# Performance work log

Measured on AMD Instinct MI355X. Metric: run time of the kernel, lower is better.

Reference implementation:

```python
import jax, jax.numpy as jnp
import numpy as np

B, T, N, C, H = 8, 96, 1024, 64, 64  # batch, in_len, nodes, hidden_dim, MLP hidden
NUM_TYPES, EMB = 3, 8
GROUPS = 4


def setup_inputs() -> dict:
    key = jax.random.key(0)
    ks = jax.random.split(key, 16)
    s = 0.05
    return {
        "x": jax.random.normal(ks[0], (B, T, 1, N), jnp.float32),
        "adj": jax.random.uniform(ks[1], (N, N), jnp.float32) / N,  # row-normalized-ish
        "node_type": jax.random.randint(ks[2], (N,), 0, NUM_TYPES),
        # input_projection: Conv1d(1, C, 1) -> per-channel scale + bias
        "w_in": jax.random.normal(ks[3], (C,), jnp.float32) * np.sqrt(2.0),
        "b_in": jnp.zeros((C,), jnp.float32),
        # GCN params
        "weights_pool": jax.random.normal(ks[4], (EMB, C, C), jnp.float32) * np.sqrt(2.0 / (EMB + C)),
        "node_emb": jax.random.normal(ks[5], (NUM_TYPES, EMB), jnp.float32) * s,
        # GroupNorm(4, C)
        "gn_w": jnp.ones((C,), jnp.float32),
        "gn_b": jnp.zeros((C,), jnp.float32),
        # ResBlock temporal MLP: Linear(T,H) then Linear(H,T)
        "w1": jax.random.normal(ks[6], (H, T), jnp.float32) * np.sqrt(1.0 / T),
        "b1": jnp.zeros((H,), jnp.float32),
        "w2": jax.random.normal(ks[7], (T, H), jnp.float32) * np.sqrt(1.0 / H),
        "b2": jnp.zeros((T,), jnp.float32),
        # out_projection: Conv1d(C, 1, 1)
        "w_out": jax.random.normal(ks[8], (C,), jnp.float32) * np.sqrt(2.0 / C),
        "b_out": jnp.zeros((), jnp.float32),
    }


def reference(x, adj, node_type, w_in, b_in, weights_pool, node_emb,
              gn_w, gn_b, w1, b1, w2, b2, w_out, b_out):
    Bx, Tx, _, Nx = x.shape
    BT = Bx * Tx
    # input_projection: Conv1d(1->C, k=1) on (BT, 1, N)
    h = x.reshape(BT, Nx)                                   # channel dim is 1
    h = h[:, None, :] * w_in[None, :, None] + b_in[None, :, None]   # (BT, C, N)
    x_in = h
    # --- GCN with adaptive per-node weights ---
    feats = jnp.swapaxes(h, 1, 2)                            # (BT, N, C)
    nt_emb = node_emb[node_type]                             # gather -> (N, 8)
    node_w = jnp.einsum('nd,dio->nio', nt_emb, weights_pool) # (N, C, C)
    feats = jnp.einsum('nm,bmi->bni', adj, feats)            # adj @ feats
    feats = jnp.einsum('bni,nio->bno', feats, node_w)        # per-node matmul
    h = jnp.swapaxes(feats, 1, 2) + x_in                     # (BT, C, N)
    # --- GroupNorm(4, C), eps=1e-5 ---
    g = h.reshape(BT, GROUPS, C // GROUPS, Nx)
    mu = g.mean(axis=(2, 3), keepdims=True)
    var = g.var(axis=(2, 3), keepdims=True)
    g = (g - mu) / jnp.sqrt(var + 1e-5)
    h = g.reshape(BT, C, Nx) * gn_w[None, :, None] + gn_b[None, :, None]
    # --- temporal mixer: (b t) c n -> (b n) t c ---
    h = h.reshape(Bx, Tx, C, Nx).transpose(0, 3, 1, 2).reshape(Bx * Nx, Tx, C)
    ht = jnp.swapaxes(h, 1, 2)                               # (BN, C, T)
    t = jax.nn.relu(ht @ w1.T + b1) @ w2.T + b2              # (BN, C, T)
    h = h + jnp.swapaxes(t, 1, 2)                            # (BN, T, C)
    # --- silu + out_projection: Conv1d(C->1, k=1) over (BN, C, T) ---
    y = jax.nn.silu(jnp.swapaxes(h, 1, 2))                   # (BN, C, T)
    y = jnp.einsum('bct,c->bt', y, w_out) + b_out            # (BN, T)
    y = y.reshape(Bx, Nx, Tx).transpose(0, 2, 1)[:, :, None, :]  # (B, T, 1, N)
    return y
```

## Files before the change

### kernel.cpp

```cpp
#include <hip/hip_runtime.h>
#include <hip/hip_bf16.h>
#include <math.h>

#define B_   8
#define T_   96
#define N_   1024
#define C_   64
#define H_   64
#define BT_  768
#define EMB_ 8

typedef __attribute__((ext_vector_type(8))) short short8v;
typedef __attribute__((ext_vector_type(4))) float f32x4;

__device__ __forceinline__ ushort f2bf(float f) {
    unsigned int u = __float_as_uint(f);
    unsigned int r = (u + 0x7fffu + ((u >> 16) & 1u)) >> 16;
    return (ushort)r;
}
__device__ __forceinline__ float bf2f(ushort h) {
    return __uint_as_float(((unsigned int)h) << 16);
}

__global__ __launch_bounds__(256) void k_setup(const float* __restrict__ wpool,
                                               const float* __restrict__ w_in,
                                               const float* __restrict__ b_in,
                                               const float* __restrict__ adj,
                                               const float* __restrict__ w1,
                                               const float* __restrict__ w2,
                                               float* __restrict__ wp1,
                                               float* __restrict__ wpb,
                                               float* __restrict__ rs,
                                               ushort* __restrict__ wfrag1,
                                               ushort* __restrict__ wfrag2) {
    int bid = blockIdx.x;
    int tid = threadIdx.x;
    if (bid == 0) {
        for (int e = tid; e < EMB_ * C_; e += 256) {
            int d = e >> 6, c = e & 63;
            float s1 = 0.f, s2 = 0.f;
            for (int i = 0; i < C_; ++i) {
                float w = wpool[(d * C_ + i) * C_ + c];
                s1 += w_in[i] * w;
                s2 += b_in[i] * w;
            }
            wp1[e] = s1;
            wpb[e] = s2;
        }
    } else if (bid == 1) {
        for (int e = tid; e < 6144; e += 256) {
            int j = e & 7, lane = (e >> 3) & 63, frag = e >> 9;
            int mt = frag / 3, k0 = frag - 3 * mt;
            int h = 16 * mt + (lane & 15);
            int t = 32 * k0 + 8 * (lane >> 4) + j;
            wfrag1[e] = f2bf(w1[h * T_ + t]);
        }
    } else if (bid == 2) {
        for (int e = tid; e < 6144; e += 256) {
            int j = e & 7, lane = (e >> 3) & 63, frag = e >> 9;
            int mt2 = frag >> 1, ks = frag & 1;
            int t = 16 * mt2 + (lane & 15);
            int h = 32 * ks + 8 * (lane >> 4) + j;
            wfrag2[e] = f2bf(w2[t * H_ + h]);
        }
    } else {
        int row = bid - 3;
        float s = 0.f;
        for (int m = tid; m < N_; m += 256) s += adj[row * N_ + m];
#pragma unroll
        for (int off = 32; off; off >>= 1) s += __shfl_down(s, off);
        __shared__ float red[4];
        if ((tid & 63) == 0) red[tid >> 6] = s;
        __syncthreads();
        if (tid == 0) rs[row] = red[0] + red[1] + red[2] + red[3];
    }
}

__global__ __launch_bounds__(256) void k_tab(const float* __restrict__ wp1,
                                             const float* __restrict__ wpb,
                                             const float* __restrict__ emb,
                                             const float* __restrict__ w_in,
                                             const float* __restrict__ b_in,
                                             float* __restrict__ WT,
                                             float* __restrict__ BTb,
                                             float* __restrict__ TAB,
                                             float* __restrict__ GG) {
    int tid = threadIdx.x;
    int wave = tid >> 6, lane = tid & 63;
    int lq = lane & 15, g = lane >> 4;
    if (wave < 3) {
        int ty = wave, c = lane;
        float w = 0.f, bb = 0.f;
#pragma unroll
        for (int d = 0; d < EMB_; ++d) {
            float ev = emb[ty * EMB_ + d];
            w += ev * wp1[d * C_ + c];
            bb += ev * wpb[d * C_ + c];
        }
        WT[ty * C_ + c] = w;
        BTb[ty * C_ + c] = bb;
        float wi = w_in[c], bi = b_in[c];
        float vals[9] = {w, bb, w * w, bb * bb, w * wi, w * bi, wi * bb, bb * bi, w * bb};
#pragma unroll
        for (int q = 0; q < 9; ++q) {
            vals[q] += __shfl_xor(vals[q], 1);
            vals[q] += __shfl_xor(vals[q], 2);
            vals[q] += __shfl_xor(vals[q], 4);
            vals[q] += __shfl_xor(vals[q], 8);
        }
        if (lq == 0) {
#pragma unroll
            for (int q = 0; q < 9; ++q) TAB[(ty * 4 + g) * 9 + q] = vals[q];
        }
    } else {
        int c = lane;
        float wi = w_in[c], bi = b_in[c];
        float v5[5] = {wi, bi, wi * wi, bi * bi, wi * bi};
#pragma unroll
        for (int q = 0; q < 5; ++q) {
            v5[q] += __shfl_xor(v5[q], 1);
            v5[q] += __shfl_xor(v5[q], 2);
            v5[q] += __shfl_xor(v5[q], 4);
            v5[q] += __shfl_xor(v5[q], 8);
        }
        if (lq == 0) {
#pragma unroll
            for (int q = 0; q < 5; ++q) GG[g * 5 + q] = v5[q];
        }
    }
}

__global__ __launch_bounds__(256, 4) void k_ax(const float* __restrict__ x,
                                               const float* __restrict__ adj,
                                               float* __restrict__ axo) {
    __shared__ ushort Xs[32 * 64];
    __shared__ ushort As[32 * 64];
    const int tid = threadIdx.x;
    const int wave = tid >> 6, lane = tid & 63;
    const int lq = lane & 15, g4 = lane >> 4;
    const int n0 = blockIdx.x * 32, m0 = blockIdx.y * 32;
    const int mi = wave >> 1, ni = wave & 1;
    const int sr = tid >> 3, sq = tid & 7;
    const int sqx = sq ^ (sr & 7);
    const int ra = 16 * mi + lq, rb = 16 * ni + lq;

    f32x4 acc = {0.f, 0.f, 0.f, 0.f};

    for (int k0 = 0; k0 < N_; k0 += 64) {
        __syncthreads();
        {
            const float* px = x + (m0 + sr) * N_ + k0 + sq * 8;
            float4 xa = *(const float4*)px;
            float4 xb = *(const float4*)(px + 4);
            union { short8v v; __hip_bfloat162 h[4]; } o;
            o.h[0] = __float22bfloat162_rn(make_float2(xa.x, xa.y));
            o.h[1] = __float22bfloat162_rn(make_float2(xa.z, xa.w));
            o.h[2] = __float22bfloat162_rn(make_float2(xb.x, xb.y));
            o.h[3] = __float22bfloat162_rn(make_float2(xb.z, xb.w));
            *(short8v*)&Xs[sr * 64 + sqx * 8] = o.v;

            const float* pa = adj + (n0 + sr) * N_ + k0 + sq * 8;
            float4 aa = *(const float4*)pa;
            float4 ab = *(const float4*)(pa + 4);
            o.h[0] = __float22bfloat162_rn(make_float2(aa.x, aa.y));
            o.h[1] = __float22bfloat162_rn(make_float2(aa.z, aa.w));
            o.h[2] = __float22bfloat162_rn(make_float2(ab.x, ab.y));
            o.h[3] = __float22bfloat162_rn(make_float2(ab.z, ab.w));
            *(short8v*)&As[sr * 64 + sqx * 8] = o.v;
        }
        __syncthreads();
#pragma unroll
        for (int ks = 0; ks < 2; ++ks) {
            short8v a = *(const short8v*)&Xs[ra * 64 + ((4 * ks + g4) ^ (ra & 7)) * 8];
            short8v bb = *(const short8v*)&As[rb * 64 + ((4 * ks + g4) ^ (rb & 7)) * 8];
            acc = __builtin_amdgcn_mfma_f32_16x16x32_bf16(a, bb, acc, 0, 0, 0);
        }
    }
#pragma unroll
    for (int r = 0; r < 4; ++r)
        axo[(m0 + 16 * mi + 4 * g4 + r) * N_ + n0 + 16 * ni + lq] = acc[r];
}

__global__ __launch_bounds__(256) void k_gn(const float* __restrict__ x,
                                            const float* __restrict__ ax,
                                            const float* __restrict__ rs,
                                            const int* __restrict__ ntype,
                                            const float* __restrict__ TAB,
                                            const float* __restrict__ GG,
                                            float* __restrict__ muT,
                                            float* __restrict__ rgT) {
    int bt = blockIdx.x;
    int tid = threadIdx.x;
    const float* axr = ax + bt * N_;
    const float* xr = x + bt * N_;
    float S[23];
#pragma unroll
    for (int q = 0; q < 23; ++q) S[q] = 0.f;
#pragma unroll
    for (int i = 0; i < 4; ++i) {
        int n = tid + 256 * i;
        float a = axr[n], xv = xr[n], r = rs[n];
        int ty = ntype[n];
        float e0 = (ty == 0) ? 1.f : 0.f;
        float e1 = (ty == 1) ? 1.f : 0.f;
        float e2 = (ty == 2) ? 1.f : 0.f;
        float a2 = a * a, axp = a * xv, ar = a * r, xrr = xv * r, r2 = r * r;
        S[0] += e0 * a;   S[1] += e1 * a;   S[2] += e2 * a;
        S[3] += e0 * r;   S[4] += e1 * r;   S[5] += e2 * r;
        S[6] += e0 * a2;  S[7] += e1 * a2;  S[8] += e2 * a2;
        S[9] += e0 * r2;  S[10] += e1 * r2; S[11] += e2 * r2;
        S[12] += e0 * axp; S[13] += e1 * axp; S[14] += e2 * axp;
        S[15] += e0 * ar; S[16] += e1 * ar; S[17] += e2 * ar;
        S[18] += e0 * xrr; S[19] += e1 * xrr; S[20] += e2 * xrr;
        S[21] += xv;      S[22] += xv * xv;
    }
#pragma unroll
    for (int q = 0; q < 23; ++q) {
#pragma unroll
        for (int off = 32; off; off >>= 1) S[q] += __shfl_down(S[q], off);
    }
    __shared__ float wred[4][23];
    __shared__ float tot[23];
    int wave = tid >> 6, lane = tid & 63;
    if (lane == 0) {
#pragma unroll
        for (int q = 0; q < 23; ++q) wred[wave][q] = S[q];
    }
    __syncthreads();
    if (tid < 23) tot[tid] = wred[0][tid] + wred[1][tid] + wred[2][tid] + wred[3][tid];
    __syncthreads();
    if (tid < 4) {
        int g = tid;
        float M = 0.f, Q = 0.f;
#pragma unroll
        for (int ty = 0; ty < 3; ++ty) {
            const float* tb = TAB + (ty * 4 + g) * 9;
            float A1v = tot[0 + ty], R1v = tot[3 + ty], A2v = tot[6 + ty];
            float R2v = tot[9 + ty], AXv = tot[12 + ty], ARv = tot[15 + ty];
            float XRv = tot[18 + ty];
            M += tb[0] * A1v + tb[1] * R1v;
            Q += tb[2] * A2v + tb[3] * R2v +
                 2.f * (tb[4] * AXv + tb[5] * A1v + tb[6] * XRv + tb[7] * R1v + tb[8] * ARv);
        }
        float Sx = tot[21], Sx2 = tot[22];
        const float* gg = GG + g * 5;
        M += gg[0] * Sx + 1024.f * gg[1];
        Q += gg[2] * Sx2 + 2.f * gg[4] * Sx + 1024.f * gg[3];
        const float inv = 1.f / 16384.f;
        float m = M * inv;
        float v = Q * inv - m * m;
        int b = bt / T_, t = bt - b * T_;
        muT[(b * 4 + g) * T_ + t] = m;
        rgT[(b * 4 + g) * T_ + t] = rsqrtf(v + 1e-5f);
    }
}

__global__ __launch_bounds__(256, 3) void k_main(const float* __restrict__ x,
                                                 const float* __restrict__ ax,
                                                 const float* __restrict__ rs,
                                                 const int* __restrict__ ntype,
                                                 const float* __restrict__ WT,
                                                 const float* __restrict__ BTb,
                                                 const float* __restrict__ muT,
                                                 const float* __restrict__ rgT,
                                                 const float* __restrict__ w_in,
                                                 const float* __restrict__ b_in,
                                                 const float* __restrict__ gn_w,
                                                 const float* __restrict__ gn_b,
                                                 const ushort* __restrict__ wfrag1,
                                                 const ushort* __restrict__ wfrag2,
                                                 const float* __restrict__ b1,
                                                 const float* __restrict__ b2,
                                                 const float* __restrict__ w_out,
                                                 const float* __restrict__ b_out,
                                                 float* __restrict__ out) {
    __shared__ ushort Hs[64 * 104];
    __shared__ ushort Hd[64 * 104];
    __shared__ float axs[96], xs[96];
    __shared__ float musT[4 * 100], rgsT[4 * 100];
    __shared__ float redp[96][4];

    const int tid = threadIdx.x;
    const int n = blockIdx.x;
    const int b = blockIdx.y;
    const int wm = tid >> 6;
    const int lane = tid & 63;
    const int lq = lane & 15;
    const int g4 = lane >> 4;

    short8v w1f[4][3], w2f[6][2];
#pragma unroll
    for (int mt = 0; mt < 4; ++mt)
#pragma unroll
        for (int k0 = 0; k0 < 3; ++k0)
            w1f[mt][k0] = *(const short8v*)(wfrag1 + (((mt * 3 + k0) << 6) + lane) * 8);
#pragma unroll
    for (int mt2 = 0; mt2 < 6; ++mt2)
#pragma unroll
        for (int ks = 0; ks < 2; ++ks)
            w2f[mt2][ks] = *(const short8v*)(wfrag2 + (((mt2 * 2 + ks) << 6) + lane) * 8);

    if (tid < 192) {
        int t = (tid < 96) ? tid : tid - 96;
        float v = (tid < 96) ? ax[(b * T_ + t) * N_ + n] : x[(b * T_ + t) * N_ + n];
        if (tid < 96) axs[t] = v; else xs[t] = v;
    }
    for (int j = tid; j < 384; j += 256) {
        int g = j / 96, t = j - 96 * g;
        musT[g * 100 + t] = muT[b * 384 + j];
        rgsT[g * 100 + t] = rgT[b * 384 + j];
    }
    __syncthreads();

    const int c = 16 * wm + lq;
    const int ty = ntype[n];
    const float rsn = rs[n];
    const float wlc = WT[ty * C_ + c];
    const float blc = BTb[ty * C_ + c];
    const float wic = w_in[c], bic = b_in[c];
    const float gwc = gn_w[c], gbc = gn_b[c];
    const float base = rsn * blc + bic;

    f32x4 acc1[4] = {{0.f, 0.f, 0.f, 0.f}, {0.f, 0.f, 0.f, 0.f},
                     {0.f, 0.f, 0.f, 0.f}, {0.f, 0.f, 0.f, 0.f}};
#pragma unroll
    for (int k0 = 0; k0 < 3; ++k0) {
        int t8 = 32 * k0 + 8 * g4;
        float4 a0 = *(const float4*)&axs[t8];
        float4 a1 = *(const float4*)&axs[t8 + 4];
        float4 x0 = *(const float4*)&xs[t8];
        float4 x1 = *(const float4*)&xs[t8 + 4];
        float4 m0 = *(const float4*)&musT[wm * 100 + t8];
        float4 m1 = *(const float4*)&musT[wm * 100 + t8 + 4];
        float4 r0 = *(const float4*)&rgsT[wm * 100 + t8];
        float4 r1 = *(const float4*)&rgsT[wm * 100 + t8 + 4];
        float vv[8];
        vv[0] = ((a0.x * wlc + x0.x * wic + base) - m0.x) * (r0.x * gwc) + gbc;
        vv[1] = ((a0.y * wlc + x0.y * wic + base) - m0.y) * (r0.y * gwc) + gbc;
        vv[2] = ((a0.z * wlc + x0.z * wic + base) - m0.z) * (r0.z * gwc) + gbc;
        vv[3] = ((a0.w * wlc + x0.w * wic + base) - m0.w) * (r0.w * gwc) + gbc;
        vv[4] = ((a1.x * wlc + x1.x * wic + base) - m1.x) * (r1.x * gwc) + gbc;
        vv[5] = ((a1.y * wlc + x1.y * wic + base) - m1.y) * (r1.y * gwc) + gbc;
        vv[6] = ((a1.z * wlc + x1.z * wic + base) - m1.z) * (r1.z * gwc) + gbc;
        vv[7] = ((a1.w * wlc + x1.w * wic + base) - m1.w) * (r1.w * gwc) + gbc;
        union { short8v v; __hip_bfloat162 h2[4]; } o;
        o.h2[0] = __float22bfloat162_rn(make_float2(vv[0], vv[1]));
        o.h2[1] = __float22bfloat162_rn(make_float2(vv[2], vv[3]));
        o.h2[2] = __float22bfloat162_rn(make_float2(vv[4], vv[5]));
        o.h2[3] = __float22bfloat162_rn(make_float2(vv[6], vv[7]));
        *(short8v*)&Hs[c * 104 + t8] = o.v;
#pragma unroll
        for (int mt = 0; mt < 4; ++mt)
            acc1[mt] = __builtin_amdgcn_mfma_f32_16x16x32_bf16(w1f[mt][k0], o.v, acc1[mt], 0, 0, 0);
    }

#pragma unroll
    for (int mt = 0; mt < 4; ++mt) {
        float4 b1v = *(const float4*)&b1[16 * mt + 4 * g4];
        __hip_bfloat162 p0 = __float22bfloat162_rn(make_float2(
            fmaxf(acc1[mt][0] + b1v.x, 0.f), fmaxf(acc1[mt][1] + b1v.y, 0.f)));
        __hip_bfloat162 p1 = __float22bfloat162_rn(make_float2(
            fmaxf(acc1[mt][2] + b1v.z, 0.f), fmaxf(acc1[mt][3] + b1v.w, 0.f)));
        union { uint2 u; __hip_bfloat162 h2[2]; } w;
        w.h2[0] = p0; w.h2[1] = p1;
        *(uint2*)&Hd[c * 104 + 16 * mt + 4 * g4] = w.u;
    }

    f32x4 acc2[6] = {{0.f, 0.f, 0.f, 0.f}, {0.f, 0.f, 0.f, 0.f},
                     {0.f, 0.f, 0.f, 0.f}, {0.f, 0.f, 0.f, 0.f},
                     {0.f, 0.f, 0.f, 0.f}, {0.f, 0.f, 0.f, 0.f}};
#pragma unroll
    for (int ks = 0; ks < 2; ++ks) {
        short8v af = *(const short8v*)&Hd[c * 104 + 32 * ks + 8 * g4];
#pragma unroll
        for (int mt2 = 0; mt2 < 6; ++mt2)
            acc2[mt2] = __builtin_amdgcn_mfma_f32_16x16x32_bf16(af, w2f[mt2][ks], acc2[mt2], 0, 0, 0);
    }

    float4 wo4 = *(const float4*)&w_out[16 * wm + 4 * g4];
#pragma unroll
    for (int mt2 = 0; mt2 < 6; ++mt2) {
        int tv = 16 * mt2 + lq;
        float bz = b2[tv];
        float pm = 0.f;
#pragma unroll
        for (int r = 0; r < 4; ++r) {
            float res = bf2f(Hs[(16 * wm + 4 * g4 + r) * 104 + tv]);
            float z = res + acc2[mt2][r] + bz;
            float sg = __builtin_amdgcn_rcpf(1.f + __expf(-z));
            pm += z * sg * wo4[r];
        }
        pm += __shfl_xor(pm, 16);
        pm += __shfl_xor(pm, 32);
        if (g4 == 0) redp[tv][wm] = pm;
    }
    __syncthreads();

    if (tid < 96) {
        float4 v = *(const float4*)&redp[tid][0];
        out[(b * T_ + tid) * N_ + n] = v.x + v.y + v.z + v.w + b_out[0];
    }
}

extern "C" void kernel_launch(void* const* d_in, const int* in_sizes, int n_in,
                              void* d_out, int out_size, void* d_ws, size_t ws_size,
                              hipStream_t stream) {
    const float* x     = (const float*)d_in[0];
    const float* adj   = (const float*)d_in[1];
    const int*   ntype = (const int*)d_in[2];
    const float* w_in  = (const float*)d_in[3];
    const float* b_in  = (const float*)d_in[4];
    const float* wpool = (const float*)d_in[5];
    const float* emb   = (const float*)d_in[6];
    const float* gn_w  = (const float*)d_in[7];
    const float* gn_b  = (const float*)d_in[8];
    const float* w1    = (const float*)d_in[9];
    const float* b1    = (const float*)d_in[10];
    const float* w2    = (const float*)d_in[11];
    const float* b2    = (const float*)d_in[12];
    const float* w_out = (const float*)d_in[13];
    const float* b_out = (const float*)d_in[14];
    float* out = (float*)d_out;
    float* ws = (float*)d_ws;

    float* wp1  = ws;
    float* wpb  = ws + 512;
    float* rsv  = ws + 1024;
    float* WT   = ws + 2048;
    float* BTb  = ws + 2240;
    float* TAB  = ws + 2432;
    float* GG   = ws + 2540;
    float* muT  = ws + 2560;
    float* rgT  = ws + 5632;
    ushort* wfrag1 = (ushort*)(ws + 8704);
    ushort* wfrag2 = (ushort*)(ws + 11776);
    float* axb  = ws + 14848;

    k_setup<<<dim3(1027), dim3(256), 0, stream>>>(wpool, w_in, b_in, adj, w1, w2,
                                                  wp1, wpb, rsv, wfrag1, wfrag2);
    k_tab<<<dim3(1), dim3(256), 0, stream>>>(wp1, wpb, emb, w_in, b_in,
                                             WT, BTb, TAB, GG);
    k_ax<<<dim3(32, 24), dim3(256), 0, stream>>>(x, adj, axb);
    k_gn<<<dim3(768), dim3(256), 0, stream>>>(x, axb, rsv, ntype, TAB, GG, muT, rgT);
    k_main<<<dim3(1024, 8), dim3(256), 0, stream>>>(x, axb, rsv, ntype, WT, BTb,
                                                    muT, rgT, w_in, b_in, gn_w, gn_b,
                                                    wfrag1, wfrag2, b1, b2,
                                                    w_out, b_out, out);
}
```

Baseline: 93.94 us.

## Process four nodes per block in k_main using transposed x and AX buffers

```diff
diff --git a/kernel.cpp b/kernel.cpp
--- a/kernel.cpp
+++ b/kernel.cpp
@@ -28,11 +28,13 @@
                                                const float* __restrict__ adj,
                                                const float* __restrict__ w1,
                                                const float* __restrict__ w2,
+                                               const float* __restrict__ x,
                                                float* __restrict__ wp1,
                                                float* __restrict__ wpb,
                                                float* __restrict__ rs,
                                                ushort* __restrict__ wfrag1,
-                                               ushort* __restrict__ wfrag2) {
+                                               ushort* __restrict__ wfrag2,
+                                               float* __restrict__ xT) {
     int bid = blockIdx.x;
     int tid = threadIdx.x;
     if (bid == 0) {
@@ -63,7 +65,7 @@
             int h = 32 * ks + 8 * (lane >> 4) + j;
             wfrag2[e] = f2bf(w2[t * H_ + h]);
         }
-    } else {
+    } else if (bid < 1027) {
         int row = bid - 3;
         float s = 0.f;
         for (int m = tid; m < N_; m += 256) s += adj[row * N_ + m];
@@ -73,6 +75,24 @@
         if ((tid & 63) == 0) red[tid >> 6] = s;
         __syncthreads();
         if (tid == 0) rs[row] = red[0] + red[1] + red[2] + red[3];
+    } else {
+        __shared__ float tile[64][65];
+        int tnum = bid - 1027;
+        int ti = tnum >> 4;
+        int tj = tnum & 15;
+#pragma unroll
+        for (int k = 0; k < 16; ++k) {
+            int idx = tid + 256 * k;
+            int r = idx >> 6, cq = idx & 63;
+            tile[r][cq] = x[(ti * 64 + r) * N_ + tj * 64 + cq];
+        }
+        __syncthreads();
+#pragma unroll
+        for (int k = 0; k < 16; ++k) {
+            int idx = tid + 256 * k;
+            int r = idx >> 6, cq = idx & 63;
+            xT[(tj * 64 + r) * BT_ + ti * 64 + cq] = tile[cq][r];
+        }
     }
 }
 
@@ -132,7 +152,8 @@
 
 __global__ __launch_bounds__(256, 4) void k_ax(const float* __restrict__ x,
                                                const float* __restrict__ adj,
-                                               float* __restrict__ axo) {
+                                               float* __restrict__ axo,
+                                               float* __restrict__ axT) {
     __shared__ ushort Xs[32 * 64];
     __shared__ ushort As[32 * 64];
     const int tid = threadIdx.x;
@@ -179,6 +200,8 @@
 #pragma unroll
     for (int r = 0; r < 4; ++r)
         axo[(m0 + 16 * mi + 4 * g4 + r) * N_ + n0 + 16 * ni + lq] = acc[r];
+    float4 tv = make_float4(acc[0], acc[1], acc[2], acc[3]);
+    *(float4*)&axT[(n0 + 16 * ni + lq) * BT_ + m0 + 16 * mi + 4 * g4] = tv;
 }
 
 __global__ __launch_bounds__(256) void k_gn(const float* __restrict__ x,
@@ -255,8 +278,8 @@
     }
 }
 
-__global__ __launch_bounds__(256, 3) void k_main(const float* __restrict__ x,
-                                                 const float* __restrict__ ax,
+__global__ __launch_bounds__(256, 4) void k_main(const float* __restrict__ xT,
+                                                 const float* __restrict__ axT,
                                                  const float* __restrict__ rs,
                                                  const int* __restrict__ ntype,
                                                  const float* __restrict__ WT,
@@ -276,12 +299,12 @@
                                                  float* __restrict__ out) {
     __shared__ ushort Hs[64 * 104];
     __shared__ ushort Hd[64 * 104];
-    __shared__ float axs[96], xs[96];
+    __shared__ float axs[4][96], xs[4][96];
     __shared__ float musT[4 * 100], rgsT[4 * 100];
-    __shared__ float redp[96][4];
+    __shared__ float redp[4][96][4];
 
     const int tid = threadIdx.x;
-    const int n = blockIdx.x;
+    const int n0 = blockIdx.x * 4;
     const int b = blockIdx.y;
     const int wm = tid >> 6;
     const int lane = tid & 63;
@@ -300,105 +323,122 @@
         for (int ks = 0; ks < 2; ++ks)
             w2f[mt2][ks] = *(const short8v*)(wfrag2 + (((mt2 * 2 + ks) << 6) + lane) * 8);
 
-    if (tid < 192) {
-        int t = (tid < 96) ? tid : tid - 96;
-        float v = (tid < 96) ? ax[(b * T_ + t) * N_ + n] : x[(b * T_ + t) * N_ + n];
-        if (tid < 96) axs[t] = v; else xs[t] = v;
+    for (int j = tid; j < 384; j += 256) {
+        int nn = j / 96, t = j - nn * 96;
+        axs[nn][t] = axT[(n0 + nn) * BT_ + b * T_ + t];
+        xs[nn][t] = xT[(n0 + nn) * BT_ + b * T_ + t];
     }
     for (int j = tid; j < 384; j += 256) {
         int g = j / 96, t = j - 96 * g;
         musT[g * 100 + t] = muT[b * 384 + j];
         rgsT[g * 100 + t] = rgT[b * 384 + j];
     }
-    __syncthreads();
 
     const int c = 16 * wm + lq;
-    const int ty = ntype[n];
-    const float rsn = rs[n];
-    const float wlc = WT[ty * C_ + c];
-    const float blc = BTb[ty * C_ + c];
     const float wic = w_in[c], bic = b_in[c];
     const float gwc = gn_w[c], gbc = gn_b[c];
-    const float base = rsn * blc + bic;
-
-    f32x4 acc1[4] = {{0.f, 0.f, 0.f, 0.f}, {0.f, 0.f, 0.f, 0.f},
-                     {0.f, 0.f, 0.f, 0.f}, {0.f, 0.f, 0.f, 0.f}};
-#pragma unroll
-    for (int k0 = 0; k0 < 3; ++k0) {
-        int t8 = 32 * k0 + 8 * g4;
-        float4 a0 = *(const float4*)&axs[t8];
-        float4 a1 = *(const float4*)&axs[t8 + 4];
-        float4 x0 = *(const float4*)&xs[t8];
-        float4 x1 = *(const float4*)&xs[t8 + 4];
-        float4 m0 = *(const float4*)&musT[wm * 100 + t8];
-        float4 m1 = *(const float4*)&musT[wm * 100 + t8 + 4];
-        float4 r0 = *(const float4*)&rgsT[wm * 100 + t8];
-        float4 r1 = *(const float4*)&rgsT[wm * 100 + t8 + 4];
-        float vv[8];
-        vv[0] = ((a0.x * wlc + x0.x * wic + base) - m0.x) * (r0.x * gwc) + gbc;
-        vv[1] = ((a0.y * wlc + x0.y * wic + base) - m0.y) * (r0.y * gwc) + gbc;
-        vv[2] = ((a0.z * wlc + x0.z * wic + base) - m0.z) * (r0.z * gwc) + gbc;
-        vv[3] = ((a0.w * wlc + x0.w * wic + base) - m0.w) * (r0.w * gwc) + gbc;
-        vv[4] = ((a1.x * wlc + x1.x * wic + base) - m1.x) * (r1.x * gwc) + gbc;
-        vv[5] = ((a1.y * wlc + x1.y * wic + base) - m1.y) * (r1.y * gwc) + gbc;
-        vv[6] = ((a1.z * wlc + x1.z * wic + base) - m1.z) * (r1.z * gwc) + gbc;
-        vv[7] = ((a1.w * wlc + x1.w * wic + base) - m1.w) * (r1.w * gwc) + gbc;
-        union { short8v v; __hip_bfloat162 h2[4]; } o;
-        o.h2[0] = __float22bfloat162_rn(make_float2(vv[0], vv[1]));
-        o.h2[1] = __float22bfloat162_rn(make_float2(vv[2], vv[3]));
-        o.h2[2] = __float22bfloat162_rn(make_float2(vv[4], vv[5]));
-        o.h2[3] = __float22bfloat162_rn(make_float2(vv[6], vv[7]));
-        *(short8v*)&Hs[c * 104 + t8] = o.v;
-#pragma unroll
-        for (int mt = 0; mt < 4; ++mt)
-            acc1[mt] = __builtin_amdgcn_mfma_f32_16x16x32_bf16(w1f[mt][k0], o.v, acc1[mt], 0, 0, 0);
-    }
-
-#pragma unroll
-    for (int mt = 0; mt < 4; ++mt) {
-        float4 b1v = *(const float4*)&b1[16 * mt + 4 * g4];
-        __hip_bfloat162 p0 = __float22bfloat162_rn(make_float2(
-            fmaxf(acc1[mt][0] + b1v.x, 0.f), fmaxf(acc1[mt][1] + b1v.y, 0.f)));
-        __hip_bfloat162 p1 = __float22bfloat162_rn(make_float2(
-            fmaxf(acc1[mt][2] + b1v.z, 0.f), fmaxf(acc1[mt][3] + b1v.w, 0.f)));
-        union { uint2 u; __hip_bfloat162 h2[2]; } w;
-        w.h2[0] = p0; w.h2[1] = p1;
-        *(uint2*)&Hd[c * 104 + 16 * mt + 4 * g4] = w.u;
-    }
-
-    f32x4 acc2[6] = {{0.f, 0.f, 0.f, 0.f}, {0.f, 0.f, 0.f, 0.f},
-                     {0.f, 0.f, 0.f, 0.f}, {0.f, 0.f, 0.f, 0.f},
-                     {0.f, 0.f, 0.f, 0.f}, {0.f, 0.f, 0.f, 0.f}};
-#pragma unroll
-    for (int ks = 0; ks < 2; ++ks) {
-        short8v af = *(const short8v*)&Hd[c * 104 + 32 * ks + 8 * g4];
-#pragma unroll
-        for (int mt2 = 0; mt2 < 6; ++mt2)
-            acc2[mt2] = __builtin_amdgcn_mfma_f32_16x16x32_bf16(af, w2f[mt2][ks], acc2[mt2], 0, 0, 0);
-    }
-
-    float4 wo4 = *(const float4*)&w_out[16 * wm + 4 * g4];
-#pragma unroll
-    for (int mt2 = 0; mt2 < 6; ++mt2) {
-        int tv = 16 * mt2 + lq;
-        float bz = b2[tv];
-        float pm = 0.f;
-#pragma unroll
-        for (int r = 0; r < 4; ++r) {
-            float res = bf2f(Hs[(16 * wm + 4 * g4 + r) * 104 + tv]);
-            float z = res + acc2[mt2][r] + bz;
-            float sg = __builtin_amdgcn_rcpf(1.f + __expf(-z));
-            pm += z * sg * wo4[r];
-        }
-        pm += __shfl_xor(pm, 16);
-        pm += __shfl_xor(pm, 32);
-        if (g4 == 0) redp[tv][wm] = pm;
-    }
+    const float wlcA[3] = {WT[c], WT[64 + c], WT[128 + c]};
+    const float blcA[3] = {BTb[c], BTb[64 + c], BTb[128 + c]};
+    float4 b1q[4];
+#pragma unroll
+    for (int mt = 0; mt < 4; ++mt) b1q[mt] = *(const float4*)&b1[16 * mt + 4 * g4];
+    float b2q[6];
+#pragma unroll
+    for (int mt2 = 0; mt2 < 6; ++mt2) b2q[mt2] = b2[16 * mt2 + lq];
+    const float4 wo4 = *(const float4*)&w_out[16 * wm + 4 * g4];
     __syncthreads();
 
+#pragma unroll 1
+    for (int nn = 0; nn < 4; ++nn) {
+        const int n = n0 + nn;
+        const int ty = ntype[n];
+        const float wlc = (ty == 0) ? wlcA[0] : (ty == 1) ? wlcA[1] : wlcA[2];
+        const float blc = (ty == 0) ? blcA[0] : (ty == 1) ? blcA[1] : blcA[2];
+        const float base = rs[n] * blc + bic;
+
+        f32x4 acc1[4] = {{0.f, 0.f, 0.f, 0.f}, {0.f, 0.f, 0.f, 0.f},
+                         {0.f, 0.f, 0.f, 0.f}, {0.f, 0.f, 0.f, 0.f}};
+#pragma unroll
+        for (int k0 = 0; k0 < 3; ++k0) {
+            int t8 = 32 * k0 + 8 * g4;
+            float4 a0 = *(const float4*)&axs[nn][t8];
+            float4 a1 = *(const float4*)&axs[nn][t8 + 4];
+            float4 x0 = *(const float4*)&xs[nn][t8];
+            float4 x1 = *(const float4*)&xs[nn][t8 + 4];
+            float4 m0 = *(const float4*)&musT[wm * 100 + t8];
+            float4 m1 = *(const float4*)&musT[wm * 100 + t8 + 4];
+            float4 r0 = *(const float4*)&rgsT[wm * 100 + t8];
+            float4 r1 = *(const float4*)&rgsT[wm * 100 + t8 + 4];
+            float vv[8];
+            vv[0] = ((a0.x * wlc + x0.x * wic + base) - m0.x) * (r0.x * gwc) + gbc;
+            vv[1] = ((a0.y * wlc + x0.y * wic + base) - m0.y) * (r0.y * gwc) + gbc;
+            vv[2] = ((a0.z * wlc + x0.z * wic + base) - m0.z) * (r0.z * gwc) + gbc;
+            vv[3] = ((a0.w * wlc + x0.w * wic + base) - m0.w) * (r0.w * gwc) + gbc;
+            vv[4] = ((a1.x * wlc + x1.x * wic + base) - m1.x) * (r1.x * gwc) + gbc;
+            vv[5] = ((a1.y * wlc + x1.y * wic + base) - m1.y) * (r1.y * gwc) + gbc;
+            vv[6] = ((a1.z * wlc + x1.z * wic + base) - m1.z) * (r1.z * gwc) + gbc;
+            vv[7] = ((a1.w * wlc + x1.w * wic + base) - m1.w) * (r1.w * gwc) + gbc;
+            union { short8v v; __hip_bfloat162 h2[4]; } o;
+            o.h2[0] = __float22bfloat162_rn(make_float2(vv[0], vv[1]));
+            o.h2[1] = __float22bfloat162_rn(make_float2(vv[2], vv[3]));
+            o.h2[2] = __float22bfloat162_rn(make_float2(vv[4], vv[5]));
+            o.h2[3] = __float22bfloat162_rn(make_float2(vv[6], vv[7]));
+            *(short8v*)&Hs[c * 104 + t8] = o.v;
+#pragma unroll
+            for (int mt = 0; mt < 4; ++mt)
+                acc1[mt] = __builtin_amdgcn_mfma_f32_16x16x32_bf16(w1f[mt][k0], o.v, acc1[mt], 0, 0, 0);
+        }
+
+#pragma unroll
+        for (int mt = 0; mt < 4; ++mt) {
+            __hip_bfloat162 p0 = __float22bfloat162_rn(make_float2(
+                fmaxf(acc1[mt][0] + b1q[mt].x, 0.f), fmaxf(acc1[mt][1] + b1q[mt].y, 0.f)));
+            __hip_bfloat162 p1 = __float22bfloat162_rn(make_float2(
+                fmaxf(acc1[mt][2] + b1q[mt].z, 0.f), fmaxf(acc1[mt][3] + b1q[mt].w, 0.f)));
+            union { uint2 u; __hip_bfloat162 h2[2]; } w;
+            w.h2[0] = p0; w.h2[1] = p1;
+            *(uint2*)&Hd[c * 104 + 16 * mt + 4 * g4] = w.u;
+        }
+
+        f32x4 acc2[6] = {{0.f, 0.f, 0.f, 0.f}, {0.f, 0.f, 0.f, 0.f},
+                         {0.f, 0.f, 0.f, 0.f}, {0.f, 0.f, 0.f, 0.f},
+                         {0.f, 0.f, 0.f, 0.f}, {0.f, 0.f, 0.f, 0.f}};
+#pragma unroll
+        for (int ks = 0; ks < 2; ++ks) {
+            short8v af = *(const short8v*)&Hd[c * 104 + 32 * ks + 8 * g4];
+#pragma unroll
+            for (int mt2 = 0; mt2 < 6; ++mt2)
+                acc2[mt2] = __builtin_amdgcn_mfma_f32_16x16x32_bf16(af, w2f[mt2][ks], acc2[mt2], 0, 0, 0);
+        }
+
+#pragma unroll
+        for (int mt2 = 0; mt2 < 6; ++mt2) {
+            int tv = 16 * mt2 + lq;
+            float pm = 0.f;
+#pragma unroll
+            for (int r = 0; r < 4; ++r) {
+                float res = bf2f(Hs[(16 * wm + 4 * g4 + r) * 104 + tv]);
+                float z = res + acc2[mt2][r] + b2q[mt2];
+                float sg = __builtin_amdgcn_rcpf(1.f + __expf(-z));
+                pm += z * sg * wo4[r];
+            }
+            pm += __shfl_xor(pm, 16);
+            pm += __shfl_xor(pm, 32);
+            if (g4 == 0) redp[nn][tv][wm] = pm;
+        }
+    }
+    __syncthreads();
+
     if (tid < 96) {
-        float4 v = *(const float4*)&redp[tid][0];
-        out[(b * T_ + tid) * N_ + n] = v.x + v.y + v.z + v.w + b_out[0];
+        float bo = b_out[0];
+        float4 y;
+        float* py = (float*)&y;
+#pragma unroll
+        for (int nn = 0; nn < 4; ++nn) {
+            float4 v = *(const float4*)&redp[nn][tid][0];
+            py[nn] = v.x + v.y + v.z + v.w + bo;
+        }
+        *(float4*)&out[(b * T_ + tid) * N_ + n0] = y;
     }
 }
 
@@ -435,15 +475,17 @@
     ushort* wfrag1 = (ushort*)(ws + 8704);
     ushort* wfrag2 = (ushort*)(ws + 11776);
     float* axb  = ws + 14848;
-
-    k_setup<<<dim3(1027), dim3(256), 0, stream>>>(wpool, w_in, b_in, adj, w1, w2,
-                                                  wp1, wpb, rsv, wfrag1, wfrag2);
+    float* axTb = ws + 14848 + 786432;
+    float* xTb  = ws + 14848 + 2 * 786432;
+
+    k_setup<<<dim3(1219), dim3(256), 0, stream>>>(wpool, w_in, b_in, adj, w1, w2, x,
+                                                  wp1, wpb, rsv, wfrag1, wfrag2, xTb);
     k_tab<<<dim3(1), dim3(256), 0, stream>>>(wp1, wpb, emb, w_in, b_in,
                                              WT, BTb, TAB, GG);
-    k_ax<<<dim3(32, 24), dim3(256), 0, stream>>>(x, adj, axb);
+    k_ax<<<dim3(32, 24), dim3(256), 0, stream>>>(x, adj, axb, axTb);
     k_gn<<<dim3(768), dim3(256), 0, stream>>>(x, axb, rsv, ntype, TAB, GG, muT, rgT);
-    k_main<<<dim3(1024, 8), dim3(256), 0, stream>>>(x, axb, rsv, ntype, WT, BTb,
-                                                    muT, rgT, w_in, b_in, gn_w, gn_b,
-                                                    wfrag1, wfrag2, b1, b2,
-                                                    w_out, b_out, out);
-}
+    k_main<<<dim3(256, 8), dim3(256), 0, stream>>>(xTb, axTb, rsv, ntype, WT, BTb,
+                                                   muT, rgT, w_in, b_in, gn_w, gn_b,
+                                                   wfrag1, wfrag2, b1, b2,
+                                                   w_out, b_out, out);
+}
```

After: 185.0 us. 1.97x slower.
